# Kernel tuning notes

Measured on AMD Instinct MI355X. Metric: run time of the kernel, lower is better.

The kernel has to match this reference:

```python
import jax, jax.numpy as jnp
import numpy as np

NV, NA, T, FD, C, E = 192, 64, 128, 1024, 128, 262144
SPK = 3
N = (NV + NA) * T  # 32768 total graph nodes
NEG = -1e30


def _seg_max(msg, dst, mask):
    # masked scatter-max; PyG fills segments with no messages with 0
    m = jnp.where(mask[:, None], msg, NEG)
    out = jax.ops.segment_max(m, dst, num_segments=N)
    return jnp.where(out > NEG * 0.5, out, 0.0)


def _edge_conv(x, src, dst, mask, W1, b1, W2, b2):
    # EdgeConv: max_j MLP(cat[x_i, x_j - x_i])
    xi = x[dst]
    h = jnp.concatenate([xi, x[src] - xi], axis=-1)  # [E, 2C]
    h = jax.nn.relu(h @ W1 + b1) @ W2 + b2
    return _seg_max(h, dst, mask)


def _sage_conv(x, src, dst, mask, Wl, bl, Wr):
    # SAGEConv: lin_l(mean_j x_j) + lin_r(x_i), lin_r has no bias
    mf = mask.astype(x.dtype)
    s = jax.ops.segment_sum(x[src] * mf[:, None], dst, num_segments=N)
    cnt = jax.ops.segment_sum(mf, dst, num_segments=N)
    mean = s / jnp.maximum(cnt, 1.0)[:, None]
    return mean @ Wl + bl + x @ Wr


def setup_inputs():
    ks = jax.random.split(jax.random.key(0), 24)
    s = 0.05
    vals = jnp.array([-3, -2, -1, 0, 1, 3], jnp.int32)
    return {
        "x_visual": jax.random.normal(ks[0], (NV, T, FD), jnp.float32),
        "x_audio": jax.random.normal(ks[1], (NA, T, FD), jnp.float32),
        "W011": jax.random.normal(ks[2], (FD, C)) * s, "b011": jnp.zeros((C,)),
        "W012": jax.random.normal(ks[3], (FD, C)) * s, "b012": jnp.zeros((C,)),
        "ecA_W1": jax.random.normal(ks[4], (2 * C, C)) * s, "ecA_b1": jnp.zeros((C,)),
        "ecA_W2": jax.random.normal(ks[5], (C, C)) * s, "ecA_b2": jnp.zeros((C,)),
        "ec1_W1": jax.random.normal(ks[6], (2 * C, C)) * s, "ec1_b1": jnp.zeros((C,)),
        "ec1_W2": jax.random.normal(ks[7], (C, C)) * s, "ec1_b2": jnp.zeros((C,)),
        "ec2_W1": jax.random.normal(ks[8], (2 * C, C)) * s, "ec2_b1": jnp.zeros((C,)),
        "ec2_W2": jax.random.normal(ks[9], (C, C)) * s, "ec2_b2": jnp.zeros((C,)),
        "ec3_W1": jax.random.normal(ks[10], (2 * C, C)) * s, "ec3_b1": jnp.zeros((C,)),
        "ec3_W2": jax.random.normal(ks[11], (C, C)) * s, "ec3_b2": jnp.zeros((C,)),
        "sage_Wl": jax.random.normal(ks[12], (C, C)) * s, "sage_bl": jnp.zeros((C,)),
        "sage_Wr": jax.random.normal(ks[13], (C, C)) * s,
        "fc_W": jax.random.normal(ks[14], (C, 1)) * s, "fc_b": jnp.zeros((1,)),
        "edge_index": jax.random.randint(ks[15], (2, E), 0, N, dtype=jnp.int32),
        "edge_attr": vals[jax.random.randint(ks[16], (E,), 0, 6)],
        "speakers": SPK,
    }


def reference(x_visual, x_audio, W011, b011, W012, b012,
              ecA_W1, ecA_b1, ecA_W2, ecA_b2,
              ec1_W1, ec1_b1, ec1_W2, ec1_b2,
              ec2_W1, ec2_b1, ec2_W2, ec2_b2,
              ec3_W1, ec3_b1, ec3_W2, ec3_b2,
              sage_Wl, sage_bl, sage_Wr, fc_W, fc_b,
              edge_index, edge_attr, speakers):
    xv = x_visual @ W011 + b011          # [NV, T, C]
    xa = x_audio @ W012 + b012           # [NA, T, C]
    x = jnp.concatenate([xv, xa], axis=0).reshape(-1, C)  # [N, C]
    src, dst = edge_index[0], edge_index[1]
    m_audio = edge_attr == -2
    m_vpa = edge_attr == -3
    m_acv = edge_attr == 3
    m1 = (edge_attr >= 0) & (edge_attr <= 1)
    m2 = (edge_attr <= 0) & (edge_attr >= -1)
    m3 = jnp.abs(edge_attr) <= 1
    # Visual_Add_Audio_GNN: max-aggregate (x_i + x_j)
    xa_g = jax.nn.relu(_seg_max(x[dst] + x[src], dst, m_vpa))
    a = jax.nn.relu(_edge_conv(xa_g, src, dst, m_audio, ecA_W1, ecA_b1, ecA_W2, ecA_b2))
    a_res = a @ fc_W + fc_b              # [N, 1] per-node audio scores
    # Audio_Weight_Add_Visual_GNN: sum-aggregate (w_j * x_j + x_i)
    wmsg = jnp.where(m_acv[:, None], a_res[src] * x[src] + x[dst], 0.0)
    xv2 = jax.nn.relu(jax.ops.segment_sum(wmsg, dst, num_segments=N))

    def branch(mask, W1, b1, W2, b2):
        h = jax.nn.relu(_edge_conv(xv2, src, dst, mask, W1, b1, W2, b2))
        return jax.nn.relu(_sage_conv(h, src, dst, mask, sage_Wl, sage_bl, sage_Wr))

    xo = (branch(m1, ec1_W1, ec1_b1, ec1_W2, ec1_b2)
          + branch(m2, ec2_W1, ec2_b1, ec2_W2, ec2_b2)
          + branch(m3, ec3_W1, ec3_b1, ec3_W2, ec3_b2))
    # gather main-speaker visual nodes
    idx = (jnp.arange(0, NV * T, speakers * T)[:, None] + jnp.arange(T)).reshape(-1)
    return xo[idx]
```

## Files before the change

### kernel.cpp

```cpp
#include <hip/hip_runtime.h>
#include <cstdint>
#include <cstddef>

#define NVv 192
#define NAa 64
#define TT 128
#define FDd 1024
#define CCc 128
#define EEe 262144
#define NNn 32768

typedef _Float16 f16x8 __attribute__((ext_vector_type(8)));
typedef float f32x4 __attribute__((ext_vector_type(4)));

#define CAP0 65536
#define CAP1 65536
#define CAP2 65536
#define CAP3 98304
#define CAP4 98304
#define CAP5 147456
#define ARENA_TOTAL (CAP0+CAP1+CAP2+CAP3+CAP4+CAP5)

__device__ __forceinline__ void eval_masks(int a, bool m[6]) {
    m[0] = (a == -3); m[1] = (a == -2); m[2] = (a == 3);
    m[3] = (a >= 0) & (a <= 1);
    m[4] = (a >= -1) & (a <= 0);
    m[5] = (a >= -1) & (a <= 1);
}

__global__ __launch_bounds__(256) void k_zero(float* __restrict__ p) {
    size_t i = (size_t)blockIdx.x * 1024 + (size_t)threadIdx.x * 4;
    *(float4*)(p + i) = make_float4(0.f, 0.f, 0.f, 0.f);
}

__global__ __launch_bounds__(256) void k_zero_need(
    const int* __restrict__ histj, const int* __restrict__ basej,
    float* __restrict__ AH)
{
    int col = threadIdx.x & 127, sub = threadIdx.x >> 7;
    for (int d = blockIdx.x * 2 + sub; d < NNn; d += gridDim.x * 2) {
        int c = histj[d];
        bool need;
        if (c == 0) need = true;
        else {
            int b = basej[d], e = b + c;
            need = ((b & 63) == 0) || ((e & 63) == 0) || ((b >> 6) != ((e - 1) >> 6));
        }
        if (need) AH[(size_t)d * 128 + col] = 0.f;
    }
}

__global__ __launch_bounds__(256) void k_wprep_big(
    const float* __restrict__ W011, const float* __restrict__ W012,
    _Float16* __restrict__ dst)
{
    int idx = blockIdx.x * 256 + threadIdx.x;
    int which = idx >> 17;
    int r = idx & 131071;
    int n = r >> 10, k = r & 1023;
    const float* src = which ? W012 : W011;
    dst[idx] = (_Float16)src[k * 128 + n];
}

struct WSmall { const float* p[14]; };

__global__ __launch_bounds__(256) void k_wprep_small(WSmall ws, _Float16* __restrict__ dst)
{
    int idx = blockIdx.x * 256 + threadIdx.x;
    int seg = idx >> 14;
    int r = idx & 16383;
    int n = r >> 7, k = r & 127;
    const float* src = ws.p[seg];
    float v = src[k * 128 + n];
    if (seg < 12 && (seg % 3) == 0) v -= src[16384 + k * 128 + n];
    dst[idx] = (_Float16)v;
}

__global__ __launch_bounds__(256) void k_hist(
    const int* __restrict__ attr, const int* __restrict__ edst,
    int* __restrict__ hist)
{
    int e = blockIdx.x * 256 + threadIdx.x;
    int a = attr[e], d = edst[e];
    bool m[6]; eval_masks(a, m);
#pragma unroll
    for (int j = 0; j < 6; ++j)
        if (m[j]) atomicAdd(&hist[j * NNn + d], 1);
}

__global__ __launch_bounds__(256) void k_scan_a(
    const int* __restrict__ hist, int* __restrict__ base, int* __restrict__ bsum)
{
    __shared__ int wsum[4];
    int bid = blockIdx.x;
    int idx = bid * 256 + threadIdx.x;
    int tid = threadIdx.x, lane = tid & 63, wv = tid >> 6;
    int v = hist[idx];
    int x = v;
#pragma unroll
    for (int off = 1; off < 64; off <<= 1) {
        int y = __shfl_up(x, off, 64);
        if (lane >= off) x += y;
    }
    if (lane == 63) wsum[wv] = x;
    __syncthreads();
    int add = 0;
    for (int w = 0; w < wv; ++w) add += wsum[w];
    base[idx] = add + x - v;
    if (tid == 255) bsum[bid] = add + x;
}

__global__ __launch_bounds__(384) void k_scan_b(int* __restrict__ bsum, int* __restrict__ cnts)
{
    int wv = threadIdx.x >> 6;
    int lane = threadIdx.x & 63;
    int run = 0;
#pragma unroll
    for (int c0 = 0; c0 < 128; c0 += 64) {
        int v = bsum[wv * 128 + c0 + lane];
        int x = v;
#pragma unroll
        for (int off = 1; off < 64; off <<= 1) {
            int y = __shfl_up(x, off, 64);
            if (lane >= off) x += y;
        }
        bsum[wv * 128 + c0 + lane] = run + (x - v);
        run += __shfl(x, 63, 64);
    }
    if (lane == 0) cnts[wv] = run;
}

__global__ __launch_bounds__(256) void k_scan_c(int* __restrict__ base, const int* __restrict__ bsum)
{
    base[blockIdx.x * 256 + threadIdx.x] += bsum[blockIdx.x];
}

__global__ __launch_bounds__(256) void k_fill(
    const int* __restrict__ esrc, const int* __restrict__ edst,
    const int* __restrict__ attr, const int* __restrict__ base,
    int* __restrict__ fill, int2* __restrict__ arena)
{
    int e = blockIdx.x * 256 + threadIdx.x;
    int a = attr[e];
    int s = esrc[e], d = edst[e];
    bool m[6]; eval_masks(a, m);
    const int caps[6] = {CAP0, CAP1, CAP2, CAP3, CAP4, CAP5};
    const int offs[6] = {0, CAP0, CAP0+CAP1, CAP0+CAP1+CAP2,
                         CAP0+CAP1+CAP2+CAP3, CAP0+CAP1+CAP2+CAP3+CAP4};
#pragma unroll
    for (int j = 0; j < 6; ++j) {
        if (m[j]) {
            int pos = base[j * NNn + d] + atomicAdd(&fill[j * NNn + d], 1);
            if (pos < caps[j]) arena[offs[j] + pos] = make_int2(s, d);
        }
    }
}

__global__ __launch_bounds__(256) void k_proj(
    const float* __restrict__ xv, const float* __restrict__ xa,
    const _Float16* __restrict__ BTv, const _Float16* __restrict__ BTa,
    const float* __restrict__ bv_, const float* __restrict__ ba_,
    float* __restrict__ X)
{
    __shared__ _Float16 Bl[128][136];
    __shared__ float bb[128];
    const int tid = threadIdx.x, wave = tid >> 6, lane = tid & 63;
    const int blk = blockIdx.x;
    const float* A; const _Float16* BT; const float* bias; int mbase, obase;
    if (blk < 384) { A = xv; BT = BTv; bias = bv_; mbase = blk * 64; obase = mbase; }
    else { A = xa; BT = BTa; bias = ba_; mbase = (blk - 384) * 64; obase = 24576 + mbase; }
    if (tid < 128) bb[tid] = bias[tid];

    const int mrow = mbase + wave * 16 + (lane & 15);
    const int fk   = (lane >> 4) * 8;
    f32x4 acc[8];
#pragma unroll
    for (int i = 0; i < 8; ++i) acc[i] = (f32x4){0,0,0,0};

    f16x8 af[4];
#pragma unroll
    for (int t4 = 0; t4 < 4; ++t4) {
        const float* asrc = A + (size_t)mrow * 1024 + t4 * 32 + fk;
        float4 a0 = *(const float4*)asrc;
        float4 a1 = *(const float4*)(asrc + 4);
        af[t4] = (f16x8){ (_Float16)a0.x, (_Float16)a0.y, (_Float16)a0.z, (_Float16)a0.w,
                          (_Float16)a1.x, (_Float16)a1.y, (_Float16)a1.z, (_Float16)a1.w };
    }

    for (int kc = 0; kc < 8; ++kc) {
        __syncthreads();
#pragma unroll
        for (int it = 0; it < 8; ++it) {
            int c = it * 256 + tid;
            int n = c >> 4, koff = (c & 15) * 8;
            *(f16x8*)&Bl[n][koff] = *(const f16x8*)(BT + (size_t)n * 1024 + kc * 128 + koff);
        }
        __syncthreads();
        f16x8 nf[4];
        if (kc < 7) {
#pragma unroll
            for (int t4 = 0; t4 < 4; ++t4) {
                const float* asrc = A + (size_t)mrow * 1024 + (kc + 1) * 128 + t4 * 32 + fk;
                float4 a0 = *(const float4*)asrc;
                float4 a1 = *(const float4*)(asrc + 4);
                nf[t4] = (f16x8){ (_Float16)a0.x, (_Float16)a0.y, (_Float16)a0.z, (_Float16)a0.w,
                                  (_Float16)a1.x, (_Float16)a1.y, (_Float16)a1.z, (_Float16)a1.w };
            }
        }
#pragma unroll
        for (int t4 = 0; t4 < 4; ++t4)
#pragma unroll
            for (int nt = 0; nt < 8; ++nt) {
                f16x8 bf = *(const f16x8*)&Bl[nt * 16 + (lane & 15)][t4 * 32 + fk];
                acc[nt] = __builtin_amdgcn_mfma_f32_16x16x32_f16(af[t4], bf, acc[nt], 0, 0, 0);
            }
#pragma unroll
        for (int t4 = 0; t4 < 4; ++t4) af[t4] = nf[t4];
    }
    __syncthreads();
    float* Hsf = (float*)&Bl[0][0] + (size_t)wave * 16 * 132;
    const int cbase = lane & 15, rloc = (lane >> 4) * 4;
#pragma unroll
    for (int nt = 0; nt < 8; ++nt) {
        int c2 = nt * 16 + cbase;
        float bvv = bb[c2];
#pragma unroll
        for (int rr = 0; rr < 4; ++rr)
            Hsf[(rloc + rr) * 132 + c2] = acc[nt][rr] + bvv;
    }
#pragma unroll
    for (int it = 0; it < 8; ++it) {
        int id = it * 64 + lane;
        int row = id >> 5, off = (id & 31) * 4;
        float4 v = *(float4*)&Hsf[row * 132 + off];
        *(float4*)&X[(size_t)(obase + wave * 16 + row) * 128 + off] = v;
    }
}

__global__ __launch_bounds__(256) void k_pv(
    const float* __restrict__ A,
    const _Float16* __restrict__ BT1, const float* __restrict__ b1,
    const _Float16* __restrict__ BT2,
    _Float16* __restrict__ P, _Float16* __restrict__ V)
{
    __shared__ _Float16 Bl1[128][136];
    __shared__ _Float16 Bl2[128][136];
    __shared__ float bb[128];
    const int tid = threadIdx.x, wave = tid >> 6, lane = tid & 63;
    const int r0 = blockIdx.x * 64 + wave * 16;

    const int fk = (lane >> 4) * 8;
    const int mrow = blockIdx.x * 64 + wave * 16 + (lane & 15);
    float4 a0[4], a1[4];
#pragma unroll
    for (int t4 = 0; t4 < 4; ++t4) {
        const float* asrc = A + (size_t)mrow * 128 + t4 * 32 + fk;
        a0[t4] = *(const float4*)asrc;
        a1[t4] = *(const float4*)(asrc + 4);
    }
#pragma unroll
    for (int it = 0; it < 8; ++it) {
        int c = it * 256 + tid;
        int n = c >> 4, koff = (c & 15) * 8;
        *(f16x8*)&Bl1[n][koff] = *(const f16x8*)(BT1 + (size_t)n * 128 + koff);
        *(f16x8*)&Bl2[n][koff] = *(const f16x8*)(BT2 + (size_t)n * 128 + koff);
    }
    if (tid < 128) bb[tid] = b1[tid];
    __syncthreads();

    f16x8 af[4];
#pragma unroll
    for (int t4 = 0; t4 < 4; ++t4)
        af[t4] = (f16x8){ (_Float16)a0[t4].x, (_Float16)a0[t4].y, (_Float16)a0[t4].z, (_Float16)a0[t4].w,
                          (_Float16)a1[t4].x, (_Float16)a1[t4].y, (_Float16)a1[t4].z, (_Float16)a1[t4].w };
    f32x4 acc1[8], acc2[8];
#pragma unroll
    for (int i = 0; i < 8; ++i) { acc1[i] = (f32x4){0,0,0,0}; acc2[i] = (f32x4){0,0,0,0}; }
#pragma unroll
    for (int t4 = 0; t4 < 4; ++t4)
#pragma unroll
        for (int nt = 0; nt < 8; ++nt) {
            f16x8 bf1 = *(const f16x8*)&Bl1[nt * 16 + (lane & 15)][t4 * 32 + fk];
            f16x8 bf2 = *(const f16x8*)&Bl2[nt * 16 + (lane & 15)][t4 * 32 + fk];
            acc1[nt] = __builtin_amdgcn_mfma_f32_16x16x32_f16(af[t4], bf1, acc1[nt], 0, 0, 0);
            acc2[nt] = __builtin_amdgcn_mfma_f32_16x16x32_f16(af[t4], bf2, acc2[nt], 0, 0, 0);
        }
    __syncthreads();
    _Float16* Hs = &Bl1[0][0] + (size_t)wave * 16 * 136;
    const int cbase = lane & 15, rloc = (lane >> 4) * 4;
#pragma unroll
    for (int nt = 0; nt < 8; ++nt) {
        int c2 = nt * 16 + cbase;
        float bvv = bb[c2];
#pragma unroll
        for (int rr = 0; rr < 4; ++rr)
            Hs[(rloc + rr) * 136 + c2] = (_Float16)(acc1[nt][rr] + bvv);
    }
#pragma unroll
    for (int it = 0; it < 4; ++it) {
        int id = it * 64 + lane;
        int row = id >> 4, koff = (id & 15) * 8;
        *(f16x8*)&P[(size_t)(r0 + row) * 128 + koff] = *(f16x8*)&Hs[row * 136 + koff];
    }
#pragma unroll
    for (int nt = 0; nt < 8; ++nt) {
        int c2 = nt * 16 + cbase;
#pragma unroll
        for (int rr = 0; rr < 4; ++rr)
            Hs[(rloc + rr) * 136 + c2] = (_Float16)acc2[nt][rr];
    }
#pragma unroll
    for (int it = 0; it < 4; ++it) {
        int id = it * 64 + lane;
        int row = id >> 4, koff = (id & 15) * 8;
        *(f16x8*)&V[(size_t)(r0 + row) * 128 + koff] = *(f16x8*)&Hs[row * 136 + koff];
    }
}

__global__ __launch_bounds__(256, 3) void k_edge_mlp(
    const _Float16* __restrict__ P, const _Float16* __restrict__ V,
    const _Float16* __restrict__ W2T, const float* __restrict__ b2,
    const int2* __restrict__ list, const int* __restrict__ cntp, int cap,
    float* __restrict__ agg)
{
    __shared__ _Float16 Rl[64][136];
    __shared__ _Float16 W2l[128][136];
    __shared__ float b2l[128];
    __shared__ int2 eSD[64];
    __shared__ unsigned char gstart[66];
    __shared__ int gdst[64];
    __shared__ int ngrS;

    int cnt = min(*cntp, cap);
    int ntiles = (cnt + 63) >> 6;
    if ((int)blockIdx.x >= ntiles) return;

    const int tid  = threadIdx.x;
    const int wave = tid >> 6;
    const int lane = tid & 63;

#pragma unroll
    for (int i = 0; i < 8; ++i) {
        int c = tid + i * 256;
        int n = c >> 4, koff = (c & 15) * 8;
        *(f16x8*)&W2l[n][koff] = *(const f16x8*)(W2T + n * 128 + koff);
    }
    if (tid < 128) b2l[tid] = b2[tid];

    const int col   = tid & 127;
    const int half  = tid >> 7;
    const int frow  = wave * 16 + (lane & 15);
    const int fq    = (lane >> 4) * 8;
    const int rbase = wave * 16 + (lane >> 4) * 4;
    const int cbase = lane & 15;
    const int rrow  = tid >> 4;
    const int rch   = (tid & 15) * 8;

    for (int t = blockIdx.x; t < ntiles; t += gridDim.x) {
        __syncthreads();
        if (tid < 64) {
            int e = t * 64 + tid;
            eSD[tid] = (e < cnt) ? list[e] : make_int2(0, -1);
        }
        __syncthreads();
        if (tid < 64) {
            int d = eSD[tid].y;
            bool flag = (tid == 0) || (d != eSD[tid - 1].y);
            unsigned long long bm = __ballot(flag);
            int rank = (int)__popcll(bm & ((1ull << tid) - 1ull));
            if (flag) { gstart[rank] = (unsigned char)tid; gdst[rank] = d; }
            if (tid == 0) {
                int ng = (int)__popcll(bm);
                ngrS = ng;
                gstart[ng] = 64;
            }
        }
#pragma unroll
        for (int p = 0; p < 4; ++p) {
            int i = p * 16 + rrow;
            int2 sd = eSD[i];
            f16x8 rv = {0, 0, 0, 0, 0, 0, 0, 0};
            if (sd.y >= 0) {
                f16x8 pv = *(const f16x8*)(P + (size_t)sd.y * 128 + rch);
                f16x8 vv = *(const f16x8*)(V + (size_t)sd.x * 128 + rch);
                rv = pv + vv;
#pragma unroll
                for (int q = 0; q < 8; ++q)
                    rv[q] = (rv[q] > (_Float16)0.f) ? rv[q] : (_Float16)0.f;
            }
            *(f16x8*)&Rl[i][rch] = rv;
        }
        __syncthreads();

        f32x4 acc[8];
#pragma unroll
        for (int i = 0; i < 8; ++i) acc[i] = (f32x4){0,0,0,0};
#pragma unroll
        for (int t4 = 0; t4 < 4; ++t4) {
            f16x8 af = *(const f16x8*)&Rl[frow][t4 * 32 + fq];
#pragma unroll
            for (int nt = 0; nt < 8; ++nt) {
                f16x8 bf = *(const f16x8*)&W2l[nt * 16 + (lane & 15)][t4 * 32 + fq];
                acc[nt] = __builtin_amdgcn_mfma_f32_16x16x32_f16(af, bf, acc[nt], 0, 0, 0);
            }
        }
        __syncthreads();
#pragma unroll
        for (int nt = 0; nt < 8; ++nt) {
            int c2 = nt * 16 + cbase;
            float bv = b2l[c2];
#pragma unroll
            for (int rr = 0; rr < 4; ++rr)
                Rl[rbase + rr][c2] = (_Float16)fmaxf(acc[nt][rr] + bv, 0.f);
        }
        __syncthreads();
        int ng = ngrS;
        for (int g = half; g < ng; g += 2) {
            int s = gstart[g], e = gstart[g + 1];
            int d = gdst[g];
            if (d < 0) continue;
            float m = 0.f;
            for (int i = s; i < e; ++i)
                m = fmaxf(m, (float)Rl[i][col]);
            size_t o = (size_t)d * 128 + col;
            if (s == 0 || e == 64)
                atomicMax((unsigned int*)&agg[o], __float_as_uint(m));
            else
                agg[o] = m;
        }
    }
}

__global__ __launch_bounds__(256) void k_csr_vpa(
    const float* __restrict__ X, const int2* __restrict__ list,
    const int* __restrict__ base, const int* __restrict__ cntarr, int cap,
    float* __restrict__ S)
{
    int col = threadIdx.x & 127;
    int sub = threadIdx.x >> 7;
    for (int d = blockIdx.x * 2 + sub; d < NNn; d += gridDim.x * 2) {
        int c = cntarr[d];
        float v = 0.f;
        if (c > 0) {
            int b = base[d];
            int end = min(b + c, cap);
            float mx = -3.0e38f;
            for (int i = b; i < end; ++i)
                mx = fmaxf(mx, X[(size_t)list[i].x * 128 + col]);
            v = fmaxf(X[(size_t)d * 128 + col] + mx, 0.f);
        }
        S[(size_t)d * 128 + col] = v;
    }
}

__global__ __launch_bounds__(256) void k_csr_acv(
    const float* __restrict__ X, const float* __restrict__ ares,
    const int2* __restrict__ list,
    const int* __restrict__ base, const int* __restrict__ cntarr, int cap,
    float* __restrict__ S)
{
    int col = threadIdx.x & 127;
    int sub = threadIdx.x >> 7;
    for (int d = blockIdx.x * 2 + sub; d < NNn; d += gridDim.x * 2) {
        int c = cntarr[d];
        float v = 0.f;
        if (c > 0) {
            int b = base[d];
            int end = min(b + c, cap);
            float s = 0.f;
            for (int i = b; i < end; ++i) {
                int sr = list[i].x;
                s += ares[sr] * X[(size_t)sr * 128 + col];
            }
            v = fmaxf(s + (float)c * X[(size_t)d * 128 + col], 0.f);
        }
        S[(size_t)d * 128 + col] = v;
    }
}

__global__ __launch_bounds__(256) void k_csr_meanc(
    const float* __restrict__ AH, const int2* __restrict__ list,
    const int* __restrict__ basej, const int* __restrict__ histj, int cap,
    const int* __restrict__ spk, int ntarg,
    float* __restrict__ S1c, float* __restrict__ AHc)
{
    int col = threadIdx.x & 127;
    int sub = threadIdx.x >> 7;
    int step = spk[0] * TT;
    for (int ci = blockIdx.x * 2 + sub; ci < ntarg; ci += gridDim.x * 2) {
        int d = (ci >> 7) * step + (ci & 127);
        int c = histj[d];
        float v = 0.f;
        if (c > 0) {
            int b = basej[d];
            int end = min(b + c, cap);
            float s = 0.f;
            for (int i = b; i < end; ++i)
                s += AH[(size_t)list[i].x * 128 + col];
            v = s / (float)c;
        }
        S1c[(size_t)ci * 128 + col] = v;
        AHc[(size_t)ci * 128 + col] = AH[(size_t)d * 128 + col];
    }
}

__global__ __launch_bounds__(256) void k_fc(
    const float* __restrict__ A, const float* __restrict__ W,
    const float* __restrict__ b, float* __restrict__ ares)
{
    int node = blockIdx.x * 4 + (threadIdx.x >> 6);
    int lane = threadIdx.x & 63;
    const float* row = A + (size_t)node * 128;
    float v = row[lane] * W[lane] + row[lane + 64] * W[lane + 64];
#pragma unroll
    for (int off = 32; off > 0; off >>= 1) v += __shfl_down(v, off, 64);
    if (lane == 0) ares[node] = v + b[0];
}

__global__ __launch_bounds__(256) void k_sage_out(
    const float* __restrict__ S1c, const float* __restrict__ AHc,
    const _Float16* __restrict__ WlT, const _Float16* __restrict__ WrT,
    const float* __restrict__ bl, float* __restrict__ out, int ntarg)
{
    __shared__ _Float16 Al[64][40];
    __shared__ _Float16 Bl[128][40];
    const int tid  = threadIdx.x;
    const int wave = tid >> 6;
    const int lane = tid & 63;
    const int m0   = blockIdx.x * 64;

    f32x4 accB[8], accO[8];
#pragma unroll
    for (int i = 0; i < 8; ++i) { accB[i] = (f32x4){0,0,0,0}; accO[i] = (f32x4){0,0,0,0}; }

    const int ar = tid >> 2;
    const int ak = (tid & 3) * 8;
    const int fr = wave * 16 + (lane & 15);
    const int fk = (lane >> 4) * 8;
    const int rbase = wave * 16 + (lane >> 4) * 4;
    const int cbase = lane & 15;

    for (int seg = 0; seg < 6; ++seg) {
        int b = seg >> 1, which = seg & 1;
        const float* A = (which ? AHc : S1c) + (size_t)b * ntarg * 128;
        const _Float16* BT = which ? WrT : WlT;
        for (int k0 = 0; k0 < 128; k0 += 32) {
            __syncthreads();
            const float* asrc = A + (size_t)(m0 + ar) * 128 + (k0 + ak);
            float4 a0 = *(const float4*)asrc;
            float4 a1 = *(const float4*)(asrc + 4);
            f16x8 av = { (_Float16)a0.x, (_Float16)a0.y, (_Float16)a0.z, (_Float16)a0.w,
                         (_Float16)a1.x, (_Float16)a1.y, (_Float16)a1.z, (_Float16)a1.w };
            *(f16x8*)&Al[ar][ak] = av;
#pragma unroll
            for (int i = 0; i < 2; ++i) {
                int c = tid + i * 256;
                int n = c >> 2, koff = (c & 3) * 8;
                *(f16x8*)&Bl[n][koff] = *(const f16x8*)(BT + (size_t)n * 128 + k0 + koff);
            }
            __syncthreads();
            f16x8 af = *(const f16x8*)&Al[fr][fk];
#pragma unroll
            for (int nt = 0; nt < 8; ++nt) {
                f16x8 bf = *(const f16x8*)&Bl[nt * 16 + (lane & 15)][fk];
                accB[nt] = __builtin_amdgcn_mfma_f32_16x16x32_f16(af, bf, accB[nt], 0, 0, 0);
            }
        }
        if (which) {
#pragma unroll
            for (int nt = 0; nt < 8; ++nt) {
                int col = nt * 16 + cbase;
                float bv = bl[col];
#pragma unroll
                for (int rr = 0; rr < 4; ++rr) {
                    accO[nt][rr] += fmaxf(accB[nt][rr] + bv, 0.f);
                    accB[nt][rr] = 0.f;
                }
            }
        }
    }
#pragma unroll
    for (int nt = 0; nt < 8; ++nt) {
        int col = nt * 16 + cbase;
#pragma unroll
        for (int rr = 0; rr < 4; ++rr)
            out[(size_t)(m0 + rbase + rr) * 128 + col] = accO[nt][rr];
    }
}

extern "C" void kernel_launch(void* const* d_in, const int* in_sizes, int n_in,
                              void* d_out, int out_size, void* d_ws, size_t ws_size,
                              hipStream_t stream)
{
    (void)in_sizes; (void)n_in; (void)ws_size;
    const float* xv   = (const float*)d_in[0];
    const float* xa   = (const float*)d_in[1];
    const float* W011 = (const float*)d_in[2];
    const float* b011 = (const float*)d_in[3];
    const float* W012 = (const float*)d_in[4];
    const float* b012 = (const float*)d_in[5];
    const float* ecW1[4] = {(const float*)d_in[6],  (const float*)d_in[10],
                            (const float*)d_in[14], (const float*)d_in[18]};
    const float* ecb1[4] = {(const float*)d_in[7],  (const float*)d_in[11],
                            (const float*)d_in[15], (const float*)d_in[19]};
    const float* ecW2[4] = {(const float*)d_in[8],  (const float*)d_in[12],
                            (const float*)d_in[16], (const float*)d_in[20]};
    const float* ecb2[4] = {(const float*)d_in[9],  (const float*)d_in[13],
                            (const float*)d_in[17], (const float*)d_in[21]};
    const float* sageWl = (const float*)d_in[22];
    const float* sagebl = (const float*)d_in[23];
    const float* sageWr = (const float*)d_in[24];
    const float* fcW    = (const float*)d_in[25];
    const float* fcb    = (const float*)d_in[26];
    const int*   esrc   = (const int*)d_in[27];
    const int*   edst   = esrc + EEe;
    const int*   attr   = (const int*)d_in[28];
    const int*   spk    = (const int*)d_in[29];
    float* out = (float*)d_out;
    const int ntarg = out_size >> 7;

    const size_t NC = (size_t)NNn * CCc;
    float* ws   = (float*)d_ws;
    float* X    = ws;
    float* S1   = ws + 1 * NC;
    float* AH   = ws + 2 * NC;
    float* XV2  = ws + 3 * NC;
    float* AHc  = ws + 4 * NC;
    _Float16* P16 = (_Float16*)(ws + 5 * NC);
    _Float16* V16 = P16 + NC;
    float* ARES = ws + 6 * NC;
    int*   cnts = (int*)(ARES + NNn);
    int*   bsum = cnts + 16;
    int*   hist = bsum + 1024;
    int*   fill = hist + 6 * NNn;
    int*   base = fill + 6 * NNn;
    int2*  arena = (int2*)(base + 6 * NNn);
    _Float16* WT = (_Float16*)(arena + ARENA_TOTAL);

    const int offs[6] = {0, CAP0, CAP0+CAP1, CAP0+CAP1+CAP2,
                         CAP0+CAP1+CAP2+CAP3, CAP0+CAP1+CAP2+CAP3+CAP4};
    const int caps[6] = {CAP0, CAP1, CAP2, CAP3, CAP4, CAP5};

    const _Float16* W011T = WT;
    const _Float16* W012T = WT + 131072;
    const _Float16* WTs   = WT + 262144;
    const _Float16* WlT   = WTs + 12 * 16384;
    const _Float16* WrT   = WTs + 13 * 16384;

    k_wprep_big<<<1024, 256, 0, stream>>>(W011, W012, WT);
    WSmall wsm;
    for (int i = 0; i < 4; ++i) {
        wsm.p[3*i + 0] = ecW1[i];
        wsm.p[3*i + 1] = ecW1[i] + 16384;
        wsm.p[3*i + 2] = ecW2[i];
    }
    wsm.p[12] = sageWl; wsm.p[13] = sageWr;
    k_wprep_small<<<896, 256, 0, stream>>>(wsm, (_Float16*)WTs);
    k_zero<<<(2 * 6 * NNn) / 1024, 256, 0, stream>>>((float*)hist);
    k_hist<<<EEe / 256, 256, 0, stream>>>(attr, edst, hist);
    k_scan_a<<<768, 256, 0, stream>>>(hist, base, bsum);
    k_scan_b<<<1, 384, 0, stream>>>(bsum, cnts);
    k_scan_c<<<768, 256, 0, stream>>>(base, bsum);
    k_fill<<<EEe / 256, 256, 0, stream>>>(esrc, edst, attr, base, fill, arena);

    k_proj<<<512, 256, 0, stream>>>(xv, xa, W011T, W012T, b011, b012, X);
    k_csr_vpa<<<2048, 256, 0, stream>>>(X, arena + offs[0], base + 0 * NNn,
                                        hist + 0 * NNn, caps[0], S1);
    k_pv<<<512, 256, 0, stream>>>(S1, WTs, ecb1[0], WTs + 16384, P16, V16);
    k_zero_need<<<2048, 256, 0, stream>>>(hist + 1 * NNn, base + 1 * NNn, AH);
    k_edge_mlp<<<2048, 256, 0, stream>>>(P16, V16, WTs + 2 * 16384, ecb2[0],
                                         arena + offs[1], cnts + 1, caps[1], AH);
    k_fc<<<NNn / 4, 256, 0, stream>>>(AH, fcW, fcb, ARES);
    k_csr_acv<<<2048, 256, 0, stream>>>(X, ARES, arena + offs[2], base + 2 * NNn,
                                        hist + 2 * NNn, caps[2], XV2);
    for (int b = 0; b < 3; ++b) {
        int j = 3 + b;
        const _Float16* Wd = WTs + (3 * (b + 1)) * 16384;
        k_pv<<<512, 256, 0, stream>>>(XV2, Wd, ecb1[b + 1], Wd + 16384, P16, V16);
        k_zero_need<<<2048, 256, 0, stream>>>(hist + j * NNn, base + j * NNn, AH);
        k_edge_mlp<<<2048, 256, 0, stream>>>(P16, V16, Wd + 2 * 16384, ecb2[b + 1],
                                             arena + offs[j], cnts + j, caps[j], AH);
        k_csr_meanc<<<2048, 256, 0, stream>>>(AH, arena + offs[j], base + j * NNn,
                                              hist + j * NNn, caps[j], spk, ntarg,
                                              S1 + (size_t)b * ntarg * 128,
                                              AHc + (size_t)b * ntarg * 128);
    }
    k_sage_out<<<ntarg / 64, 256, 0, stream>>>(S1, AHc, WlT, WrT, sagebl, out, ntarg);
}
```

Before: 568.5 us.

## Split projection GEMM along K into two halves with a separate reduce kernel

The input projection kernel now uses 512-thread blocks covering 128 rows each, and every tile is split into two K halves handled by separate blocks. Partial sums go to two scratch buffers, which reuse the XV2 and AH arrays. A new elementwise kernel then adds the two partials and the bias into X. The aim is more parallelism per tile and shorter per-block K loops. The cost is an extra launch and a write-then-read round trip for two full fp32 partial buffers.

```diff
diff --git a/kernel.cpp b/kernel.cpp
--- a/kernel.cpp
+++ b/kernel.cpp
@@ -156,20 +156,19 @@
     }
 }
 
-__global__ __launch_bounds__(256) void k_proj(
+__global__ __launch_bounds__(512) void k_proj(
     const float* __restrict__ xv, const float* __restrict__ xa,
     const _Float16* __restrict__ BTv, const _Float16* __restrict__ BTa,
-    const float* __restrict__ bv_, const float* __restrict__ ba_,
-    float* __restrict__ X)
+    float* __restrict__ Pp0, float* __restrict__ Pp1)
 {
     __shared__ _Float16 Bl[128][136];
-    __shared__ float bb[128];
     const int tid = threadIdx.x, wave = tid >> 6, lane = tid & 63;
-    const int blk = blockIdx.x;
-    const float* A; const _Float16* BT; const float* bias; int mbase, obase;
-    if (blk < 384) { A = xv; BT = BTv; bias = bv_; mbase = blk * 64; obase = mbase; }
-    else { A = xa; BT = BTa; bias = ba_; mbase = (blk - 384) * 64; obase = 24576 + mbase; }
-    if (tid < 128) bb[tid] = bias[tid];
+    const int tile = blockIdx.x >> 1, kh = blockIdx.x & 1;
+    const float* A; const _Float16* BT; int mbase, obase;
+    if (tile < 192) { A = xv; BT = BTv; mbase = tile * 128; obase = mbase; }
+    else { A = xa; BT = BTa; mbase = (tile - 192) * 128; obase = 24576 + mbase; }
+    float* Pout = kh ? Pp1 : Pp0;
+    const int kbase = kh * 512;
 
     const int mrow = mbase + wave * 16 + (lane & 15);
     const int fk   = (lane >> 4) * 8;
@@ -180,27 +179,28 @@
     f16x8 af[4];
 #pragma unroll
     for (int t4 = 0; t4 < 4; ++t4) {
-        const float* asrc = A + (size_t)mrow * 1024 + t4 * 32 + fk;
+        const float* asrc = A + (size_t)mrow * 1024 + kbase + t4 * 32 + fk;
         float4 a0 = *(const float4*)asrc;
         float4 a1 = *(const float4*)(asrc + 4);
         af[t4] = (f16x8){ (_Float16)a0.x, (_Float16)a0.y, (_Float16)a0.z, (_Float16)a0.w,
                           (_Float16)a1.x, (_Float16)a1.y, (_Float16)a1.z, (_Float16)a1.w };
     }
 
-    for (int kc = 0; kc < 8; ++kc) {
+    for (int kc = 0; kc < 4; ++kc) {
         __syncthreads();
 #pragma unroll
-        for (int it = 0; it < 8; ++it) {
-            int c = it * 256 + tid;
+        for (int it = 0; it < 4; ++it) {
+            int c = it * 512 + tid;
             int n = c >> 4, koff = (c & 15) * 8;
-            *(f16x8*)&Bl[n][koff] = *(const f16x8*)(BT + (size_t)n * 1024 + kc * 128 + koff);
+            *(f16x8*)&Bl[n][koff] =
+                *(const f16x8*)(BT + (size_t)n * 1024 + kbase + kc * 128 + koff);
         }
         __syncthreads();
         f16x8 nf[4];
-        if (kc < 7) {
+        if (kc < 3) {
 #pragma unroll
             for (int t4 = 0; t4 < 4; ++t4) {
-                const float* asrc = A + (size_t)mrow * 1024 + (kc + 1) * 128 + t4 * 32 + fk;
+                const float* asrc = A + (size_t)mrow * 1024 + kbase + (kc + 1) * 128 + t4 * 32 + fk;
                 float4 a0 = *(const float4*)asrc;
                 float4 a1 = *(const float4*)(asrc + 4);
                 nf[t4] = (f16x8){ (_Float16)a0.x, (_Float16)a0.y, (_Float16)a0.z, (_Float16)a0.w,
@@ -218,23 +218,47 @@
         for (int t4 = 0; t4 < 4; ++t4) af[t4] = nf[t4];
     }
     __syncthreads();
-    float* Hsf = (float*)&Bl[0][0] + (size_t)wave * 16 * 132;
     const int cbase = lane & 15, rloc = (lane >> 4) * 4;
-#pragma unroll
-    for (int nt = 0; nt < 8; ++nt) {
-        int c2 = nt * 16 + cbase;
-        float bvv = bb[c2];
-#pragma unroll
-        for (int rr = 0; rr < 4; ++rr)
-            Hsf[(rloc + rr) * 132 + c2] = acc[nt][rr] + bvv;
-    }
-#pragma unroll
-    for (int it = 0; it < 8; ++it) {
-        int id = it * 64 + lane;
-        int row = id >> 5, off = (id & 31) * 4;
-        float4 v = *(float4*)&Hsf[row * 132 + off];
-        *(float4*)&X[(size_t)(obase + wave * 16 + row) * 128 + off] = v;
-    }
+    const int wgrp = wave & 3;
+    float* Hsf = (float*)&Bl[0][0] + (size_t)wgrp * 16 * 132;
+#pragma unroll
+    for (int grp = 0; grp < 2; ++grp) {
+        if ((wave >> 2) == grp) {
+#pragma unroll
+            for (int nt = 0; nt < 8; ++nt) {
+                int c2 = nt * 16 + cbase;
+#pragma unroll
+                for (int rr = 0; rr < 4; ++rr)
+                    Hsf[(rloc + rr) * 132 + c2] = acc[nt][rr];
+            }
+#pragma unroll
+            for (int it = 0; it < 8; ++it) {
+                int id = it * 64 + lane;
+                int row = id >> 5, off = (id & 31) * 4;
+                float4 v = *(float4*)&Hsf[row * 132 + off];
+                *(float4*)&Pout[(size_t)(obase + wave * 16 + row) * 128 + off] = v;
+            }
+        }
+        __syncthreads();
+    }
+}
+
+__global__ __launch_bounds__(256) void k_reduce(
+    const float* __restrict__ Pp0, const float* __restrict__ Pp1,
+    const float* __restrict__ b011, const float* __restrict__ b012,
+    float* __restrict__ X)
+{
+    size_t f = (size_t)blockIdx.x * 256 + threadIdx.x;
+    size_t i = f * 4;
+    int col = (int)(i & 127);
+    int row = (int)(i >> 7);
+    const float* bias = (row < 24576) ? b011 : b012;
+    float4 a = *(const float4*)(Pp0 + i);
+    float4 b = *(const float4*)(Pp1 + i);
+    float4 bb = *(const float4*)(bias + col);
+    float4 o = make_float4(a.x + b.x + bb.x, a.y + b.y + bb.y,
+                           a.z + b.z + bb.z, a.w + b.w + bb.w);
+    *(float4*)(X + i) = o;
 }
 
 __global__ __launch_bounds__(256) void k_pv(
@@ -663,7 +687,8 @@
     k_scan_c<<<768, 256, 0, stream>>>(base, bsum);
     k_fill<<<EEe / 256, 256, 0, stream>>>(esrc, edst, attr, base, fill, arena);
 
-    k_proj<<<512, 256, 0, stream>>>(xv, xa, W011T, W012T, b011, b012, X);
+    k_proj<<<512, 512, 0, stream>>>(xv, xa, W011T, W012T, XV2, AH);
+    k_reduce<<<(int)(NC / 1024), 256, 0, stream>>>(XV2, AH, b011, b012, X);
     k_csr_vpa<<<2048, 256, 0, stream>>>(X, arena + offs[0], base + 0 * NNn,
                                         hist + 0 * NNn, caps[0], S1);
     k_pv<<<512, 256, 0, stream>>>(S1, WTs, ecb1[0], WTs + 16384, P16, V16);
```

Measured after the change: 559.9 us. Within noise of the previous version (-1.5%).
